# Kernel tuning notes

Measured on AMD Instinct MI355X. Metric: run time of the kernel, lower is better.

Reference implementation:

```python
import math
import jax, jax.numpy as jnp
import numpy as np

N, L, W = 64, 128, 256          # batch, num windows, window size
D, H, NL = 384, 8, 4            # d_model, heads, transformer layers
DFF = 1536
CH = [1, 4, 16, 64]             # conv channels (multiplier 4)
K = 7                            # conv kernel, pad 3, stride 1; pool k2 s2
LIN_IN = 64 * 32                # cnn_linear_size = 2048


def _pe(l, d):
    pos = np.arange(l)[:, None].astype(np.float32)
    i = np.arange(d // 2)[None, :].astype(np.float32)
    ang = pos / np.power(10000.0, 2.0 * i / d)
    pe = np.zeros((l, d), np.float32)
    pe[:, 0::2] = np.sin(ang)
    pe[:, 1::2] = np.cos(ang)
    return jnp.asarray(pe)


def _conv1d(x, w, b):
    y = jax.lax.conv_general_dilated(x, w, window_strides=(1,), padding=[(3, 3)],
                                     dimension_numbers=('NCH', 'OIH', 'NCH'))
    return y + b[None, :, None]


def _maxpool2(x):
    return jax.lax.reduce_window(x, -jnp.inf, jax.lax.max, (1, 1, 2), (1, 1, 2), 'VALID')


def _ln(x, g, b):
    m = x.mean(-1, keepdims=True)
    v = ((x - m) ** 2).mean(-1, keepdims=True)
    return (x - m) * jax.lax.rsqrt(v + 1e-5) * g + b


def setup_inputs() -> dict:
    key = jax.random.key(0)
    ks = iter(jax.random.split(key, 40))
    s = 0.02
    d = {'x': jax.random.normal(next(ks), (N, L, W), jnp.float32)}
    for i in range(3):
        d[f'conv_w{i}'] = jax.random.normal(next(ks), (CH[i + 1], CH[i], K), jnp.float32) * s
        d[f'conv_b{i}'] = jnp.zeros((CH[i + 1],), jnp.float32)
    d['embed_w'] = jax.random.normal(next(ks), (LIN_IN, D), jnp.float32) * s
    d['embed_b'] = jnp.zeros((D,), jnp.float32)
    for nm, sh in [('Wq', (NL, D, D)), ('Wk', (NL, D, D)), ('Wv', (NL, D, D)), ('Wo', (NL, D, D)),
                   ('W1', (NL, D, DFF)), ('W2', (NL, DFF, D))]:
        d[nm] = jax.random.normal(next(ks), sh, jnp.float32) * s
    for nm, sh in [('bq', (NL, D)), ('bk', (NL, D)), ('bv', (NL, D)), ('bo', (NL, D)),
                   ('b1', (NL, DFF)), ('b2', (NL, D))]:
        d[nm] = jnp.zeros(sh, jnp.float32)
    d['g1'] = jnp.ones((NL, D), jnp.float32); d['be1'] = jnp.zeros((NL, D), jnp.float32)
    d['g2'] = jnp.ones((NL, D), jnp.float32); d['be2'] = jnp.zeros((NL, D), jnp.float32)
    d['cls_w'] = jax.random.normal(next(ks), (D, 1), jnp.float32) * s
    d['cls_b'] = jnp.zeros((1,), jnp.float32)
    return d


def reference(x, conv_w0, conv_b0, conv_w1, conv_b1, conv_w2, conv_b2,
              embed_w, embed_b, Wq, bq, Wk, bk, Wv, bv, Wo, bo,
              W1, b1, W2, b2, g1, be1, g2, be2, cls_w, cls_b):
    n, l, w = x.shape
    # ---- CNN window encoder: each window -> d_model token ----
    h = x.reshape(n * l, 1, w)
    for cw, cb in ((conv_w0, conv_b0), (conv_w1, conv_b1), (conv_w2, conv_b2)):
        h = _maxpool2(jax.nn.relu(_conv1d(h, cw, cb)))
    h = h.reshape(n * l, -1)                      # (N*L, cnn_linear_size)
    h = jax.nn.relu(h @ embed_w + embed_b)        # (N*L, D)
    t = h.reshape(n, l, D) + _pe(l, D)
    # ---- transformer encoder (fast_transformers post-norm layers) ----
    E = D // H
    temp = 1.0 / math.sqrt(E)
    for i in range(Wq.shape[0]):
        q = (t @ Wq[i] + bq[i]).reshape(n, l, H, E)
        k = (t @ Wk[i] + bk[i]).reshape(n, l, H, E)
        v = (t @ Wv[i] + bv[i]).reshape(n, l, H, E)
        A = jax.nn.softmax(temp * jnp.einsum('nlhe,nshe->nhls', q, k), axis=-1)
        o = jnp.einsum('nhls,nshd->nlhd', A, v).reshape(n, l, D)
        t = _ln(t + o @ Wo[i] + bo[i], g1[i], be1[i])
        y = jax.nn.relu(t @ W1[i] + b1[i]) @ W2[i] + b2[i]
        t = _ln(t + y, g2[i], be2[i])
    # ---- classifier head: mean pool over windows -> logit ----
    return t.mean(axis=1) @ cls_w + cls_b          # (N, 1)
```

## Files before the change

### kernel.cpp

```cpp
#include <hip/hip_runtime.h>
#include <math.h>


typedef float f32x4 __attribute__((ext_vector_type(4)));
typedef short bf16x8 __attribute__((ext_vector_type(8)));
typedef short s16x4 __attribute__((ext_vector_type(4)));

__device__ __forceinline__ short f2bf(float f) {
    union { float f; unsigned u; } c; c.f = f;
    unsigned r = (c.u + 0x7FFFu + ((c.u >> 16) & 1u)) >> 16;
    return (short)r;
}
__device__ __forceinline__ float bf2f(short s) {
    union { unsigned u; float f; } c;
    c.u = ((unsigned)(unsigned short)s) << 16;
    return c.f;
}

__device__ __forceinline__ void gload_lds16(const void* g, void* l) {
    __builtin_amdgcn_global_load_lds(
        (const __attribute__((address_space(1))) unsigned int*)g,
        (__attribute__((address_space(3))) unsigned int*)l,
        16, 0, 0);
}

__global__ __launch_bounds__(256) void prep_kernel(
    const float* __restrict__ ew,
    const float* __restrict__ Wq, const float* __restrict__ Wk,
    const float* __restrict__ Wv, const float* __restrict__ Wo,
    const float* __restrict__ W1, const float* __restrict__ W2,
    const float* __restrict__ bq, const float* __restrict__ bk,
    const float* __restrict__ bv, const float* __restrict__ w2,
    short* __restrict__ ewT, short* __restrict__ WqkvT,
    short* __restrict__ WoT, short* __restrict__ W1T,
    short* __restrict__ W2T, float* __restrict__ pe,
    float* __restrict__ bqkv, short* __restrict__ w2T)
{
    __shared__ float tile[32][33];
    int id = blockIdx.x;
    int tid = threadIdx.x;
    int tx = tid & 31, ty = tid >> 5;

    const float* Wp;
    short* Wtp;
    int K, N, kb, nb;

    if (id < 768) {
        K = 2048; N = 384;
        kb = (id & 63) * 32; nb = (id >> 6) * 32;
        Wp = ew; Wtp = ewT;
    } else if (id < 2496) {
        int t = id - 768;
        int kbi = t % 12, nbi = (t / 12) % 12, z = t / 144;
        int layer = z / 3, which = z - layer * 3;
        K = 384; N = 384; kb = kbi * 32; nb = nbi * 32;
        Wp = (which == 0 ? Wq : (which == 1 ? Wk : Wv)) + (size_t)layer * 147456;
        Wtp = WqkvT + (size_t)layer * 442368 + (size_t)which * 147456;
    } else if (id < 3072) {
        int t = id - 2496;
        int kbi = t % 12, nbi = (t / 12) % 12, z = t / 144;
        K = 384; N = 384; kb = kbi * 32; nb = nbi * 32;
        Wp = Wo + (size_t)z * 147456; Wtp = WoT + (size_t)z * 147456;
    } else if (id < 5376) {
        int t = id - 3072;
        int kbi = t % 12, nbi = (t / 12) % 48, z = t / 576;
        K = 384; N = 1536; kb = kbi * 32; nb = nbi * 32;
        Wp = W1 + (size_t)z * 589824; Wtp = W1T + (size_t)z * 589824;
    } else if (id < 7680) {
        int t = id - 5376;
        int kbi = t % 48, nbi = (t / 48) % 12, z = t / 576;
        K = 1536; N = 384; kb = kbi * 32; nb = nbi * 32;
        Wp = W2 + (size_t)z * 589824; Wtp = W2T + (size_t)z * 589824;
    } else if (id < 7872) {
        int idx = (id - 7680) * 256 + tid;
        int l = idx / 384, d = idx - l * 384;
        int i2 = d >> 1;
        float ang = (float)l * expf(-(2.0f * (float)i2 / 384.0f) * 9.210340371976184f);
        pe[idx] = (d & 1) ? cosf(ang) : sinf(ang);
        return;
    } else if (id < 7890) {
        int idx = (id - 7872) * 256 + tid;
        int l = idx / 1152, j3 = idx - l * 1152;
        int which = j3 / 384, j = j3 - which * 384;
        const float* b = (which == 0 ? bq : (which == 1 ? bk : bv));
        bqkv[idx] = b[l * 384 + j];
        return;
    } else {
        int idx = (id - 7890) * 256 + tid;
        int c = idx >> 7, r = idx & 127;
        int pr = r >> 5, q = (r >> 3) & 3, j = r & 7;
        int ci = (q & 1) * 8 + j;
        int sft = 2 * pr + (q >> 1);
        w2T[idx] = (sft < 7) ? f2bf(w2[c * 112 + ci * 7 + sft]) : (short)0;
        return;
    }

    #pragma unroll
    for (int r = ty; r < 32; r += 8)
        tile[r][tx] = Wp[(size_t)(kb + r) * N + nb + tx];
    __syncthreads();
    #pragma unroll
    for (int r = ty; r < 32; r += 8)
        Wtp[(size_t)(nb + r) * K + kb + tx] = f2bf(tile[tx][r]);
}

__global__ __launch_bounds__(256, 4) void cnn_kernel(
    const float* __restrict__ x,
    const float* __restrict__ w0, const float* __restrict__ b0,
    const float* __restrict__ w1, const float* __restrict__ b1,
    const short* __restrict__ w2T, const float* __restrict__ b2,
    short* __restrict__ feat)
{
    __shared__ __align__(16) char smem[26880];
    float* xs  = (float*)smem;
    float* p0  = (float*)(smem + 4224);
    short* p1T = (short*)(smem + 13056);

    int tid = threadIdx.x;
    int w = tid >> 6, lane = tid & 63;
    size_t win = (size_t)blockIdx.x * 4 + w;
    int cq = lane >> 4, cl = lane & 15;

    float* xs_w = xs + w * 264;
    float* p0_w = p0 + w * 552;
    short* p1T_w = p1T + w * 1728;

    int ca = lane & 3;
    int cb = lane & 15, g = lane >> 4;
    float w0r[7], w1r[4][7];
    float b0r = b0[ca];
    float b1r = b1[cb];
    #pragma unroll
    for (int k = 0; k < 7; ++k) w0r[k] = w0[ca * 7 + k];
    #pragma unroll
    for (int ci = 0; ci < 4; ++ci)
        #pragma unroll
        for (int k = 0; k < 7; ++k) w1r[ci][k] = w1[(cb * 4 + ci) * 7 + k];

    {
        f32x4 v = *(const f32x4*)(x + win * 256 + lane * 4);
        *(f32x4*)&xs_w[4 + lane * 4] = v;
        if (lane < 2) *(f32x4*)&xs_w[lane * 260] = (f32x4){0.f, 0.f, 0.f, 0.f};
    }

    {
        int pa = lane >> 2;
        #pragma unroll
        for (int t2 = 0; t2 < 8; ++t2) {
            int pp = t2 * 16 + pa;
            float rv[9];
            #pragma unroll
            for (int u = 0; u < 9; ++u) rv[u] = xs_w[2 * pp + u + 1];
            float a0 = b0r, a1 = b0r;
            #pragma unroll
            for (int k = 0; k < 7; ++k) {
                a0 = fmaf(w0r[k], rv[k], a0);
                a1 = fmaf(w0r[k], rv[k + 1], a1);
            }
            p0_w[ca * 138 + pp + 3] = fmaxf(fmaxf(a0, a1), 0.f);
        }
        if (lane < 4) {
            p0_w[lane * 138 + 0] = 0.f;
            p0_w[lane * 138 + 1] = 0.f;
            p0_w[lane * 138 + 2] = 0.f;
            p0_w[lane * 138 + 131] = 0.f;
            p0_w[lane * 138 + 132] = 0.f;
            p0_w[lane * 138 + 133] = 0.f;
        }
    }

    #pragma unroll
    for (int cc = 0; cc < 4; ++cc) {
        int cci = (cc + g) & 3;
        int j0 = g * 32 + cci * 8;
        float acc[8];
        #pragma unroll
        for (int m = 0; m < 8; ++m) acc[m] = b1r;
        #pragma unroll
        for (int ci = 0; ci < 4; ++ci) {
            float rv[14];
            #pragma unroll
            for (int u = 0; u < 14; ++u) rv[u] = p0_w[ci * 138 + j0 + u];
            #pragma unroll
            for (int k = 0; k < 7; ++k) {
                float ww = w1r[ci][k];
                #pragma unroll
                for (int m = 0; m < 8; ++m) acc[m] = fmaf(ww, rv[m + k], acc[m]);
            }
        }
        int po = g * 16 + cci * 4;
        #pragma unroll
        for (int m = 0; m < 4; ++m)
            p1T_w[(3 + po + m) * 24 + cb] =
                f2bf(fmaxf(fmaxf(acc[2 * m], acc[2 * m + 1]), 0.f));
    }
    {
        int* pz = (int*)p1T_w;
        if (lane < 36) pz[lane] = 0;
        if (lane < 60) pz[804 + lane] = 0;
    }
    __syncthreads();

    f32x4 acc[4][4];
    #pragma unroll
    for (int v = 0; v < 4; ++v)
        #pragma unroll
        for (int mt = 0; mt < 4; ++mt)
            acc[v][mt] = (f32x4){0.f, 0.f, 0.f, 0.f};

    {
        const short* bpb = p1T + (w * 16 + cl + (cq >> 1)) * 24 + (cq & 1) * 8;
        #pragma unroll
        for (int pr = 0; pr < 4; ++pr) {
            bf16x8 bfr[4];
            #pragma unroll
            for (int v = 0; v < 4; ++v)
                bfr[v] = *(const bf16x8*)&bpb[v * 1728 + pr * 48];
            #pragma unroll
            for (int mt = 0; mt < 4; ++mt) {
                bf16x8 af = *(const bf16x8*)&w2T[(mt * 16 + cl) * 128 +
                                                 pr * 32 + cq * 8];
                #pragma unroll
                for (int v = 0; v < 4; ++v)
                    acc[v][mt] = __builtin_amdgcn_mfma_f32_16x16x32_bf16(
                        af, bfr[v], acc[v][mt], 0, 0, 0);
            }
        }
    }

    int iev = (w * 16 + cl) >> 1;
    #pragma unroll
    for (int v = 0; v < 4; ++v) {
        short* fp = feat + ((size_t)blockIdx.x * 4 + v) * 2048;
        #pragma unroll
        for (int mt = 0; mt < 4; ++mt) {
            #pragma unroll
            for (int rg = 0; rg < 4; ++rg) {
                float vv = acc[v][mt][rg];
                float v2 = __shfl_xor(vv, 1, 64);
                if ((cl & 1) == 0) {
                    int c = mt * 16 + cq * 4 + rg;
                    float pv = fmaxf(fmaxf(vv, v2) + b2[c], 0.f);
                    fp[c * 32 + iev] = f2bf(pv);
                }
            }
        }
    }
}

template <int EPI>
__global__ __launch_bounds__(256) void gemm_bf16(
    const short* __restrict__ A, const short* __restrict__ Bt,
    const float* __restrict__ bias, const float* __restrict__ resid,
    const float* __restrict__ pe, float* __restrict__ outF,
    short* __restrict__ outB, int M, int N, int K)
{
    __shared__ short As[2][128 * 64];
    __shared__ short Bs[2][64 * 64];
    int tid = threadIdx.x;
    int w = tid >> 6, lane = tid & 63;
    int wm = w >> 1, wn = w & 1;
    int m0 = blockIdx.y * 128, n0 = blockIdx.x * 64;

    int rl = lane >> 3, sl = lane & 7;
    int cb = sl ^ rl;
    const short* aptr[4];
    const short* bptr[2];
    int arow[4], brow[2];
    #pragma unroll
    for (int l = 0; l < 4; ++l) {
        arow[l] = l * 32 + w * 8;
        aptr[l] = A + (size_t)(m0 + arow[l] + rl) * K + cb * 8;
    }
    #pragma unroll
    for (int l = 0; l < 2; ++l) {
        brow[l] = l * 32 + w * 8;
        bptr[l] = Bt + (size_t)(n0 + brow[l] + rl) * K + cb * 8;
    }

    int cq = lane >> 4, cl = lane & 15;
    f32x4 acc[4][2];
    #pragma unroll
    for (int mt = 0; mt < 4; ++mt)
        #pragma unroll
        for (int nt = 0; nt < 2; ++nt)
            acc[mt][nt] = (f32x4){0.f, 0.f, 0.f, 0.f};

    #pragma unroll
    for (int l = 0; l < 4; ++l) { gload_lds16(aptr[l], &As[0][arow[l] * 64]); aptr[l] += 64; }
    #pragma unroll
    for (int l = 0; l < 2; ++l) { gload_lds16(bptr[l], &Bs[0][brow[l] * 64]); bptr[l] += 64; }
    __syncthreads();

    int nk = K >> 6;
    for (int k = 0; k < nk; ++k) {
        int cur = k & 1;
        if (k + 1 < nk) {
            #pragma unroll
            for (int l = 0; l < 4; ++l) { gload_lds16(aptr[l], &As[cur ^ 1][arow[l] * 64]); aptr[l] += 64; }
            #pragma unroll
            for (int l = 0; l < 2; ++l) { gload_lds16(bptr[l], &Bs[cur ^ 1][brow[l] * 64]); bptr[l] += 64; }
        }
        #pragma unroll
        for (int s = 0; s < 2; ++s) {
            bf16x8 afr[4], bfr[2];
            #pragma unroll
            for (int mt = 0; mt < 4; ++mt) {
                int r = wm * 64 + mt * 16 + cl;
                int slot = (s * 4 + cq) ^ (r & 7);
                afr[mt] = *(const bf16x8*)&As[cur][r * 64 + slot * 8];
            }
            #pragma unroll
            for (int nt = 0; nt < 2; ++nt) {
                int r = wn * 32 + nt * 16 + cl;
                int slot = (s * 4 + cq) ^ (r & 7);
                bfr[nt] = *(const bf16x8*)&Bs[cur][r * 64 + slot * 8];
            }
            #pragma unroll
            for (int mt = 0; mt < 4; ++mt)
                #pragma unroll
                for (int nt = 0; nt < 2; ++nt)
                    acc[mt][nt] = __builtin_amdgcn_mfma_f32_16x16x32_bf16(
                        afr[mt], bfr[nt], acc[mt][nt], 0, 0, 0);
        }
        __syncthreads();
    }

    #pragma unroll
    for (int mt = 0; mt < 4; ++mt) {
        #pragma unroll
        for (int nt = 0; nt < 2; ++nt) {
            int col = n0 + wn * 32 + nt * 16 + cl;
            float bb = bias[col];
            #pragma unroll
            for (int rg = 0; rg < 4; ++rg) {
                int row = m0 + wm * 64 + mt * 16 + cq * 4 + rg;
                float v = acc[mt][nt][rg] + bb;
                if (EPI & 1) v = fmaxf(v, 0.f);
                if (EPI & 4) v += pe[(row & 127) * 384 + col];
                if (EPI & 2) v += resid[(size_t)row * N + col];
                if (EPI & 8) outF[(size_t)row * N + col] = v;
                if (EPI & 16) outB[(size_t)row * N + col] = f2bf(v);
            }
        }
    }
}

__global__ __launch_bounds__(512) void gemm_ln(
    const short* __restrict__ A, const short* __restrict__ Bt,
    const float* __restrict__ bias, const float* resid,
    const float* __restrict__ g, const float* __restrict__ be,
    float* t, short* __restrict__ tb, int K)
{
    __shared__ __align__(16) char smem[106496];
    short* As0 = (short*)smem;
    short* Bs0 = (short*)(smem + 8192);

    int tid = threadIdx.x;
    int w = tid >> 6, lane = tid & 63;
    int m0 = blockIdx.x * 32;
    int rl = lane >> 3, sl = lane & 7;
    int cb = sl ^ rl;

    const short* aptr = A + (size_t)(m0 + (w & 3) * 8 + rl) * K + cb * 8;
    const short* bptr[6];
    #pragma unroll
    for (int l = 0; l < 6; ++l)
        bptr[l] = Bt + (size_t)(w * 48 + l * 8 + rl) * K + cb * 8;

    int cq = lane >> 4, cl = lane & 15;
    f32x4 acc[2][3];
    #pragma unroll
    for (int mt = 0; mt < 2; ++mt)
        #pragma unroll
        for (int nt = 0; nt < 3; ++nt)
            acc[mt][nt] = (f32x4){0.f, 0.f, 0.f, 0.f};

    if (w < 4) { gload_lds16(aptr, &As0[(w * 8) * 64]); aptr += 64; }
    #pragma unroll
    for (int l = 0; l < 6; ++l) {
        gload_lds16(bptr[l], &Bs0[(w * 48 + l * 8) * 64]);
        bptr[l] += 64;
    }
    __syncthreads();

    int nk = K >> 6;
    for (int k = 0; k < nk; ++k) {
        int cur = k & 1;
        if (k + 1 < nk) {
            if (w < 4) { gload_lds16(aptr, &As0[(cur ^ 1) * 2048 + (w * 8) * 64]); aptr += 64; }
            #pragma unroll
            for (int l = 0; l < 6; ++l) {
                gload_lds16(bptr[l], &Bs0[(cur ^ 1) * 24576 + (w * 48 + l * 8) * 64]);
                bptr[l] += 64;
            }
        }
        const short* As = As0 + cur * 2048;
        const short* Bs = Bs0 + cur * 24576;
        #pragma unroll
        for (int s = 0; s < 2; ++s) {
            bf16x8 afr[2], bfr[3];
            #pragma unroll
            for (int mt = 0; mt < 2; ++mt) {
                int r = mt * 16 + cl;
                int slot = (s * 4 + cq) ^ (r & 7);
                afr[mt] = *(const bf16x8*)&As[r * 64 + slot * 8];
            }
            #pragma unroll
            for (int nt = 0; nt < 3; ++nt) {
                int r = w * 48 + nt * 16 + cl;
                int slot = (s * 4 + cq) ^ (r & 7);
                bfr[nt] = *(const bf16x8*)&Bs[r * 64 + slot * 8];
            }
            #pragma unroll
            for (int mt = 0; mt < 2; ++mt)
                #pragma unroll
                for (int nt = 0; nt < 3; ++nt)
                    acc[mt][nt] = __builtin_amdgcn_mfma_f32_16x16x32_bf16(
                        afr[mt], bfr[nt], acc[mt][nt], 0, 0, 0);
        }
        __syncthreads();
    }

    float* yb = (float*)smem;
    #pragma unroll
    for (int mt = 0; mt < 2; ++mt) {
        #pragma unroll
        for (int nt = 0; nt < 3; ++nt) {
            int col = w * 48 + nt * 16 + cl;
            float bb = bias[col];
            #pragma unroll
            for (int rg = 0; rg < 4; ++rg) {
                int rloc = mt * 16 + cq * 4 + rg;
                yb[rloc * 388 + col] =
                    acc[mt][nt][rg] + bb + resid[(size_t)(m0 + rloc) * 384 + col];
            }
        }
    }
    __syncthreads();

    int rloc = tid >> 4, sub = tid & 15;
    f32x4 vals[6];
    float s = 0.f, s2 = 0.f;
    #pragma unroll
    for (int m = 0; m < 6; ++m) {
        f32x4 vv = *(const f32x4*)&yb[rloc * 388 + m * 64 + sub * 4];
        vals[m] = vv;
        #pragma unroll
        for (int j = 0; j < 4; ++j) {
            s += vv[j];
            s2 = fmaf(vv[j], vv[j], s2);
        }
    }
    s += __shfl_xor(s, 1, 64);  s2 += __shfl_xor(s2, 1, 64);
    s += __shfl_xor(s, 2, 64);  s2 += __shfl_xor(s2, 2, 64);
    s += __shfl_xor(s, 4, 64);  s2 += __shfl_xor(s2, 4, 64);
    s += __shfl_xor(s, 8, 64);  s2 += __shfl_xor(s2, 8, 64);
    float mean = s * (1.f / 384.f);
    float var = s2 * (1.f / 384.f) - mean * mean;
    float inv = rsqrtf(var + 1e-5f);

    size_t ro = (size_t)(m0 + rloc) * 384;
    #pragma unroll
    for (int m = 0; m < 6; ++m) {
        int c0 = m * 64 + sub * 4;
        f32x4 gg = *(const f32x4*)&g[c0];
        f32x4 bb = *(const f32x4*)&be[c0];
        f32x4 ov;
        s16x4 ob2;
        #pragma unroll
        for (int j = 0; j < 4; ++j) {
            float v = (vals[m][j] - mean) * inv * gg[j] + bb[j];
            ov[j] = v;
            ob2[j] = f2bf(v);
        }
        *(f32x4*)&t[ro + c0] = ov;
        *(s16x4*)&tb[ro + c0] = ob2;
    }
}

__global__ __launch_bounds__(512) void ffn_ln(
    const short* __restrict__ A,
    const short* __restrict__ W1t,
    const short* __restrict__ W2t,
    const float* __restrict__ b1,
    const float* __restrict__ bias2,
    const float* resid,
    const float* __restrict__ g, const float* __restrict__ be,
    float* t, short* __restrict__ tb)
{
    __shared__ __align__(16) char smem[126976];
    short* Ats = (short*)smem;
    short* WsA = (short*)(smem + 24576);
    short* WsB = (short*)(smem + 73728);
    short* Hs  = (short*)(smem + 122880);

    int tid = threadIdx.x;
    int w = tid >> 6, lane = tid & 63;
    int m0 = blockIdx.x * 32;
    int rl = lane >> 3, sl = lane & 7;
    int cb = sl ^ rl;
    int cq = lane >> 4, cl = lane & 15;
    int mt = w & 1, nth = w >> 1;

    if (w < 4) {
        #pragma unroll
        for (int kc = 0; kc < 6; ++kc)
            gload_lds16(A + (size_t)(m0 + w * 8 + rl) * 384 + kc * 64 + cb * 8,
                        &Ats[(kc * 32 + w * 8) * 64]);
    }
    #pragma unroll
    for (int kc = 0; kc < 6; ++kc)
        gload_lds16(W1t + (size_t)(w * 8 + rl) * 384 + kc * 64 + cb * 8,
                    &WsA[(kc * 64 + w * 8) * 64]);
    __syncthreads();

    f32x4 yacc[2][3];
    #pragma unroll
    for (int m2 = 0; m2 < 2; ++m2)
        #pragma unroll
        for (int nt = 0; nt < 3; ++nt)
            yacc[m2][nt] = (f32x4){0.f, 0.f, 0.f, 0.f};

    for (int c = 0; c < 24; ++c) {
        #pragma unroll
        for (int l = 0; l < 6; ++l)
            gload_lds16(W2t + (size_t)(w * 48 + l * 8 + rl) * 1536 + c * 64 + cb * 8,
                        &WsB[(w * 48 + l * 8) * 64]);

        f32x4 hacc = (f32x4){0.f, 0.f, 0.f, 0.f};
        #pragma unroll
        for (int kc = 0; kc < 6; ++kc) {
            #pragma unroll
            for (int s = 0; s < 2; ++s) {
                int ra = mt * 16 + cl;
                int sa = (s * 4 + cq) ^ (ra & 7);
                bf16x8 af = *(const bf16x8*)&Ats[(kc * 32 + ra) * 64 + sa * 8];
                int rb = nth * 16 + cl;
                int sb = (s * 4 + cq) ^ (rb & 7);
                bf16x8 bf = *(const bf16x8*)&WsA[(kc * 64 + rb) * 64 + sb * 8];
                hacc = __builtin_amdgcn_mfma_f32_16x16x32_bf16(af, bf, hacc, 0, 0, 0);
            }
        }
        {
            int lc = nth * 16 + cl;
            float bb = b1[c * 64 + lc];
            int sgrp = (lc >> 3);
            #pragma unroll
            for (int rg = 0; rg < 4; ++rg) {
                int row = mt * 16 + cq * 4 + rg;
                float v = fmaxf(hacc[rg] + bb, 0.f);
                Hs[row * 64 + (sgrp ^ (row & 7)) * 8 + (lc & 7)] = f2bf(v);
            }
        }
        __syncthreads();

        if (c + 1 < 24) {
            #pragma unroll
            for (int kc = 0; kc < 6; ++kc)
                gload_lds16(W1t + (size_t)((c + 1) * 64 + w * 8 + rl) * 384 + kc * 64 + cb * 8,
                            &WsA[(kc * 64 + w * 8) * 64]);
        }
        #pragma unroll
        for (int s = 0; s < 2; ++s) {
            bf16x8 haf[2], wbf[3];
            #pragma unroll
            for (int m2 = 0; m2 < 2; ++m2) {
                int r = m2 * 16 + cl;
                int slot = (s * 4 + cq) ^ (r & 7);
                haf[m2] = *(const bf16x8*)&Hs[r * 64 + slot * 8];
            }
            #pragma unroll
            for (int nt = 0; nt < 3; ++nt) {
                int r = w * 48 + nt * 16 + cl;
                int slot = (s * 4 + cq) ^ (r & 7);
                wbf[nt] = *(const bf16x8*)&WsB[r * 64 + slot * 8];
            }
            #pragma unroll
            for (int m2 = 0; m2 < 2; ++m2)
                #pragma unroll
                for (int nt = 0; nt < 3; ++nt)
                    yacc[m2][nt] = __builtin_amdgcn_mfma_f32_16x16x32_bf16(
                        haf[m2], wbf[nt], yacc[m2][nt], 0, 0, 0);
        }
        __syncthreads();
    }

    float* yb = (float*)smem;
    #pragma unroll
    for (int m2 = 0; m2 < 2; ++m2) {
        #pragma unroll
        for (int nt = 0; nt < 3; ++nt) {
            int col = w * 48 + nt * 16 + cl;
            float bb = bias2[col];
            #pragma unroll
            for (int rg = 0; rg < 4; ++rg) {
                int rloc = m2 * 16 + cq * 4 + rg;
                yb[rloc * 388 + col] =
                    yacc[m2][nt][rg] + bb + resid[(size_t)(m0 + rloc) * 384 + col];
            }
        }
    }
    __syncthreads();

    int rloc = tid >> 4, sub = tid & 15;
    f32x4 vals[6];
    float s = 0.f, s2 = 0.f;
    #pragma unroll
    for (int m = 0; m < 6; ++m) {
        f32x4 vv = *(const f32x4*)&yb[rloc * 388 + m * 64 + sub * 4];
        vals[m] = vv;
        #pragma unroll
        for (int j = 0; j < 4; ++j) {
            s += vv[j];
            s2 = fmaf(vv[j], vv[j], s2);
        }
    }
    s += __shfl_xor(s, 1, 64);  s2 += __shfl_xor(s2, 1, 64);
    s += __shfl_xor(s, 2, 64);  s2 += __shfl_xor(s2, 2, 64);
    s += __shfl_xor(s, 4, 64);  s2 += __shfl_xor(s2, 4, 64);
    s += __shfl_xor(s, 8, 64);  s2 += __shfl_xor(s2, 8, 64);
    float mean = s * (1.f / 384.f);
    float var = s2 * (1.f / 384.f) - mean * mean;
    float inv = rsqrtf(var + 1e-5f);

    size_t ro = (size_t)(m0 + rloc) * 384;
    #pragma unroll
    for (int m = 0; m < 6; ++m) {
        int c0 = m * 64 + sub * 4;
        f32x4 gg = *(const f32x4*)&g[c0];
        f32x4 bb = *(const f32x4*)&be[c0];
        f32x4 ov;
        s16x4 ob2;
        #pragma unroll
        for (int j = 0; j < 4; ++j) {
            float v = (vals[m][j] - mean) * inv * gg[j] + bb[j];
            ov[j] = v;
            ob2[j] = f2bf(v);
        }
        *(f32x4*)&t[ro + c0] = ov;
        *(s16x4*)&tb[ro + c0] = ob2;
    }
}

__global__ __launch_bounds__(256) void qkvattn_kernel(
    const short* __restrict__ A, const short* __restrict__ Bt,
    const float* __restrict__ bias, short* __restrict__ o)
{
    __shared__ __align__(16) char smem[76544];
    short* As0 = (short*)smem;
    short* Bs0 = (short*)(smem + 32768);
    short* Qs  = (short*)smem;
    short* Ks  = (short*)(smem + 14336);
    short* Vt  = (short*)(smem + 28672);
    short* P   = (short*)(smem + 41728);

    int tid = threadIdx.x;
    int w = tid >> 6, lane = tid & 63;
    int cq = lane >> 4, cl = lane & 15;
    int n = blockIdx.x >> 3, h = blockIdx.x & 7;
    int m0 = n * 128;

    int rl = lane >> 3, sl = lane & 7;
    int cb = sl ^ rl;
    const short* aptr[4];
    int arow[4];
    #pragma unroll
    for (int l = 0; l < 4; ++l) {
        arow[l] = l * 32 + w * 8;
        aptr[l] = A + (size_t)(m0 + arow[l] + rl) * 384 + cb * 8;
    }
    const short* bptr[5];
    int brow[5];
    #pragma unroll
    for (int l = 0; l < 5; ++l) {
        brow[l] = (l < 4) ? (l * 32 + w * 8) : (128 + w * 8);
        int r = brow[l] + rl;
        int g0 = (r >= 96) ? 2 : ((r >= 48) ? 1 : 0);
        int loc = r - g0 * 48;
        bptr[l] = Bt + (size_t)(g0 * 384 + h * 48 + loc) * 384 + cb * 8;
    }

    f32x4 acc[2][9];
    #pragma unroll
    for (int mt = 0; mt < 2; ++mt)
        #pragma unroll
        for (int nt = 0; nt < 9; ++nt)
            acc[mt][nt] = (f32x4){0.f, 0.f, 0.f, 0.f};

    #pragma unroll
    for (int l = 0; l < 4; ++l) { gload_lds16(aptr[l], &As0[arow[l] * 64]); aptr[l] += 64; }
    #pragma unroll
    for (int l = 0; l < 5; ++l) {
        if (l < 4 || w < 2) { gload_lds16(bptr[l], &Bs0[brow[l] * 64]); }
        bptr[l] += 64;
    }
    __syncthreads();

    for (int k = 0; k < 6; ++k) {
        int cur = k & 1;
        if (k + 1 < 6) {
            #pragma unroll
            for (int l = 0; l < 4; ++l) {
                gload_lds16(aptr[l], &As0[(cur ^ 1) * 8192 + arow[l] * 64]);
                aptr[l] += 64;
            }
            #pragma unroll
            for (int l = 0; l < 5; ++l) {
                if (l < 4 || w < 2)
                    gload_lds16(bptr[l], &Bs0[(cur ^ 1) * 9216 + brow[l] * 64]);
                bptr[l] += 64;
            }
        }
        const short* Asb = As0 + cur * 8192;
        const short* Bsb = Bs0 + cur * 9216;
        #pragma unroll
        for (int s = 0; s < 2; ++s) {
            bf16x8 afr[2], bfr[9];
            #pragma unroll
            for (int mt = 0; mt < 2; ++mt) {
                int r = w * 32 + mt * 16 + cl;
                int slot = (s * 4 + cq) ^ (r & 7);
                afr[mt] = *(const bf16x8*)&Asb[r * 64 + slot * 8];
            }
            #pragma unroll
            for (int nt = 0; nt < 9; ++nt) {
                int r = nt * 16 + cl;
                int slot = (s * 4 + cq) ^ (r & 7);
                bfr[nt] = *(const bf16x8*)&Bsb[r * 64 + slot * 8];
            }
            #pragma unroll
            for (int mt = 0; mt < 2; ++mt)
                #pragma unroll
                for (int nt = 0; nt < 9; ++nt)
                    acc[mt][nt] = __builtin_amdgcn_mfma_f32_16x16x32_bf16(
                        afr[mt], bfr[nt], acc[mt][nt], 0, 0, 0);
        }
        __syncthreads();
    }

    const float* bh = bias + h * 48;
    #pragma unroll
    for (int mt = 0; mt < 2; ++mt) {
        #pragma unroll
        for (int nt = 0; nt < 9; ++nt) {
            int grp = nt / 3;
            int col = (nt - grp * 3) * 16 + cl;
            float bb = bh[grp * 384 + col];
            if (grp == 2) {
                int row0 = w * 32 + mt * 16 + cq * 4;
                s16x4 pv;
                #pragma unroll
                for (int rg = 0; rg < 4; ++rg) pv[rg] = f2bf(acc[mt][nt][rg] + bb);
                *(s16x4*)&Vt[col * 136 + row0] = pv;
            } else {
                short* dst = (grp == 0) ? Qs : Ks;
                #pragma unroll
                for (int rg = 0; rg < 4; ++rg) {
                    int row = w * 32 + mt * 16 + cq * 4 + rg;
                    dst[row * 56 + col] = f2bf(acc[mt][nt][rg] + bb);
                }
            }
        }
    }
    __syncthreads();

    const bf16x8 zf = (bf16x8){0, 0, 0, 0, 0, 0, 0, 0};
    bf16x8 qf[2][2];
    #pragma unroll
    for (int mt = 0; mt < 2; ++mt) {
        int r = w * 32 + mt * 16 + cl;
        qf[mt][0] = *(const bf16x8*)&Qs[r * 56 + cq * 8];
        qf[mt][1] = (cq < 2) ? *(const bf16x8*)&Qs[r * 56 + 32 + cq * 8] : zf;
    }

    f32x4 sacc[2][8];
    #pragma unroll
    for (int mt = 0; mt < 2; ++mt)
        #pragma unroll
        for (int kt = 0; kt < 8; ++kt)
            sacc[mt][kt] = (f32x4){0.f, 0.f, 0.f, 0.f};

    #pragma unroll
    for (int kt = 0; kt < 8; ++kt) {
        int r = kt * 16 + cl;
        bf16x8 kf0 = *(const bf16x8*)&Ks[r * 56 + cq * 8];
        bf16x8 kf1 = (cq < 2) ? *(const bf16x8*)&Ks[r * 56 + 32 + cq * 8] : zf;
        #pragma unroll
        for (int mt = 0; mt < 2; ++mt) {
            sacc[mt][kt] = __builtin_amdgcn_mfma_f32_16x16x32_bf16(
                qf[mt][0], kf0, sacc[mt][kt], 0, 0, 0);
            sacc[mt][kt] = __builtin_amdgcn_mfma_f32_16x16x32_bf16(
                qf[mt][1], kf1, sacc[mt][kt], 0, 0, 0);
        }
    }

    const float temp = 0.14433756729740643f;
    short* Pw = P + w * 4352;
    float denom[2][4];
    #pragma unroll
    for (int mt = 0; mt < 2; ++mt) {
        #pragma unroll
        for (int rg = 0; rg < 4; ++rg) {
            float mx = sacc[mt][0][rg];
            #pragma unroll
            for (int kt = 1; kt < 8; ++kt) mx = fmaxf(mx, sacc[mt][kt][rg]);
            mx = fmaxf(mx, __shfl_xor(mx, 1, 64));
            mx = fmaxf(mx, __shfl_xor(mx, 2, 64));
            mx = fmaxf(mx, __shfl_xor(mx, 4, 64));
            mx = fmaxf(mx, __shfl_xor(mx, 8, 64));
            int row = mt * 16 + cq * 4 + rg;
            float se = 0.f;
            #pragma unroll
            for (int kt = 0; kt < 8; ++kt) {
                float p = __expf(temp * (sacc[mt][kt][rg] - mx));
                se += p;
                Pw[row * 136 + kt * 16 + cl] = f2bf(p);
            }
            se += __shfl_xor(se, 1, 64);
            se += __shfl_xor(se, 2, 64);
            se += __shfl_xor(se, 4, 64);
            se += __shfl_xor(se, 8, 64);
            denom[mt][rg] = se;
        }
    }

    f32x4 oacc[2][3];
    #pragma unroll
    for (int mt = 0; mt < 2; ++mt)
        #pragma unroll
        for (int nt = 0; nt < 3; ++nt)
            oacc[mt][nt] = (f32x4){0.f, 0.f, 0.f, 0.f};

    #pragma unroll
    for (int ks = 0; ks < 4; ++ks) {
        bf16x8 paf[2];
        #pragma unroll
        for (int mt = 0; mt < 2; ++mt)
            paf[mt] = *(const bf16x8*)&Pw[(mt * 16 + cl) * 136 + ks * 32 + cq * 8];
        #pragma unroll
        for (int nt = 0; nt < 3; ++nt) {
            bf16x8 vf = *(const bf16x8*)&Vt[(nt * 16 + cl) * 136 + ks * 32 + cq * 8];
            #pragma unroll
            for (int mt = 0; mt < 2; ++mt)
                oacc[mt][nt] = __builtin_amdgcn_mfma_f32_16x16x32_bf16(
                    paf[mt], vf, oacc[mt][nt], 0, 0, 0);
        }
    }

    #pragma unroll
    for (int mt = 0; mt < 2; ++mt) {
        #pragma unroll
        for (int rg = 0; rg < 4; ++rg) {
            float inv = 1.f / denom[mt][rg];
            int qrow = w * 32 + mt * 16 + cq * 4 + rg;
            short* op = o + ((size_t)n * 128 + qrow) * 384 + h * 48;
            #pragma unroll
            for (int nt = 0; nt < 3; ++nt)
                op[nt * 16 + cl] = f2bf(oacc[mt][nt][rg] * inv);
        }
    }
}

__global__ __launch_bounds__(384) void head_kernel(
    const float* __restrict__ t, const float* __restrict__ cls_w,
    const float* __restrict__ cls_b, float* __restrict__ out)
{
    int n = blockIdx.x, d = threadIdx.x;
    float s = 0.f;
    for (int l = 0; l < 128; ++l) s += t[((size_t)n * 128 + l) * 384 + d];
    float p = s * (1.f / 128.f) * cls_w[d];
    #pragma unroll
    for (int off = 32; off > 0; off >>= 1) p += __shfl_xor(p, off, 64);
    __shared__ float red[6];
    if ((threadIdx.x & 63) == 0) red[threadIdx.x >> 6] = p;
    __syncthreads();
    if (threadIdx.x == 0) {
        float tot = red[0] + red[1] + red[2] + red[3] + red[4] + red[5];
        out[n] = tot + cls_b[0];
    }
}

extern "C" void kernel_launch(void* const* d_in, const int* in_sizes, int n_in,
                              void* d_out, int out_size, void* d_ws, size_t ws_size,
                              hipStream_t stream) {
    (void)n_in; (void)out_size; (void)ws_size;
    const float* x   = (const float*)d_in[0];
    const float* cw0 = (const float*)d_in[1];
    const float* cb0 = (const float*)d_in[2];
    const float* cw1 = (const float*)d_in[3];
    const float* cb1 = (const float*)d_in[4];
    const float* cw2 = (const float*)d_in[5];
    const float* cb2 = (const float*)d_in[6];
    const float* ew  = (const float*)d_in[7];
    const float* eb  = (const float*)d_in[8];
    bool dict_order = (in_sizes[10] == 589824);
    const float *Wq, *Wk, *Wv, *Wo, *W1, *W2, *bq, *bk, *bv, *bo, *b1, *b2;
    if (dict_order) {
        Wq = (const float*)d_in[9];  Wk = (const float*)d_in[10];
        Wv = (const float*)d_in[11]; Wo = (const float*)d_in[12];
        W1 = (const float*)d_in[13]; W2 = (const float*)d_in[14];
        bq = (const float*)d_in[15]; bk = (const float*)d_in[16];
        bv = (const float*)d_in[17]; bo = (const float*)d_in[18];
        b1 = (const float*)d_in[19]; b2 = (const float*)d_in[20];
    } else {
        Wq = (const float*)d_in[9];  bq = (const float*)d_in[10];
        Wk = (const float*)d_in[11]; bk = (const float*)d_in[12];
        Wv = (const float*)d_in[13]; bv = (const float*)d_in[14];
        Wo = (const float*)d_in[15]; bo = (const float*)d_in[16];
        W1 = (const float*)d_in[17]; b1 = (const float*)d_in[18];
        W2 = (const float*)d_in[19]; b2 = (const float*)d_in[20];
    }
    const float* g1  = (const float*)d_in[21];
    const float* be1 = (const float*)d_in[22];
    const float* g2  = (const float*)d_in[23];
    const float* be2 = (const float*)d_in[24];
    const float* clw = (const float*)d_in[25];
    const float* clb = (const float*)d_in[26];

    char* wp = (char*)d_ws;
    float* pe    = (float*)wp; wp += 196608;
    short* featb = (short*)wp; wp += 33554432;
    float* t     = (float*)wp; wp += 12582912;
    short* tb    = (short*)wp; wp += 6291456;
    short* qkvb  = (short*)wp; wp += 18874368;
    short* ob    = (short*)wp; wp += 6291456;
    short* ewT   = (short*)wp; wp += 1572864;
    short* WqkvT = (short*)wp; wp += 3538944;
    short* WoT   = (short*)wp; wp += 1179648;
    short* W1T   = (short*)wp; wp += 4718592;
    short* W2T   = (short*)wp; wp += 4718592;
    float* bqkv  = (float*)wp; wp += 18432;
    short* w2T   = (short*)wp; wp += 16384;
    (void)qkvb;

    const int ROWS = 8192;

    prep_kernel<<<7922, 256, 0, stream>>>(ew, Wq, Wk, Wv, Wo, W1, W2,
                                          bq, bk, bv, cw2,
                                          ewT, WqkvT, WoT, W1T, W2T,
                                          pe, bqkv, w2T);
    cnn_kernel<<<2048, 256, 0, stream>>>(x, cw0, cb0, cw1, cb1, w2T, cb2, featb);

    gemm_bf16<29><<<dim3(6, 64), 256, 0, stream>>>(featb, ewT, eb, nullptr, pe,
                                                   t, tb, ROWS, 384, 2048);
    for (int i = 0; i < 4; ++i) {
        const short* WqkvTi = WqkvT + (size_t)i * 442368;
        const short* WoTi = WoT + (size_t)i * 147456;
        const short* W1Ti = W1T + (size_t)i * 589824;
        const short* W2Ti = W2T + (size_t)i * 589824;
        qkvattn_kernel<<<512, 256, 0, stream>>>(tb, WqkvTi, bqkv + i * 1152, ob);
        gemm_ln<<<256, 512, 0, stream>>>(ob, WoTi, bo + i * 384, t,
            g1 + i * 384, be1 + i * 384, t, tb, 384);
        ffn_ln<<<256, 512, 0, stream>>>(tb, W1Ti, W2Ti, b1 + i * 1536,
            b2 + i * 384, t, g2 + i * 384, be2 + i * 384, t, tb);
    }
    head_kernel<<<64, 384, 0, stream>>>(t, clw, clb, (float*)d_out);
}
```

Measured before the change: 573.5 us.

## Software-pipeline fused FFN kernel with multi-buffered weight tiles and register-held A

```diff
diff --git a/kernel.cpp b/kernel.cpp
--- a/kernel.cpp
+++ b/kernel.cpp
@@ -489,30 +489,48 @@
     const float* __restrict__ g, const float* __restrict__ be,
     float* t, short* __restrict__ tb)
 {
-    __shared__ __align__(16) char smem[126976];
-    short* Ats = (short*)smem;
-    short* WsA = (short*)(smem + 24576);
-    short* WsB = (short*)(smem + 73728);
+    __shared__ __align__(16) char smem[128000];
+    short* WsA = (short*)smem;
+    short* WsB = (short*)(smem + 49152);
     short* Hs  = (short*)(smem + 122880);
 
     int tid = threadIdx.x;
     int w = tid >> 6, lane = tid & 63;
     int m0 = blockIdx.x * 32;
-    int rl = lane >> 3, sl = lane & 7;
-    int cb = sl ^ rl;
     int cq = lane >> 4, cl = lane & 15;
-    int mt = w & 1, nth = w >> 1;
-
+    int rl8 = lane >> 3, sl8 = lane & 7;
+    int cb8 = sl8 ^ rl8;
+    int rl16 = lane >> 2, sl4 = lane & 3;
+    int cb4 = sl4 ^ ((rl16 >> 1) & 3);
+    int mt = w & 1, nt2 = (w >> 1) & 1;
+
+    bf16x8 afr[12];
     if (w < 4) {
+        const short* ap = A + (size_t)(m0 + mt * 16 + cl) * 384;
         #pragma unroll
         for (int kc = 0; kc < 6; ++kc)
-            gload_lds16(A + (size_t)(m0 + w * 8 + rl) * 384 + kc * 64 + cb * 8,
-                        &Ats[(kc * 32 + w * 8) * 64]);
-    }
-    #pragma unroll
-    for (int kc = 0; kc < 6; ++kc)
-        gload_lds16(W1t + (size_t)(w * 8 + rl) * 384 + kc * 64 + cb * 8,
-                    &WsA[(kc * 64 + w * 8) * 64]);
+            #pragma unroll
+            for (int s = 0; s < 2; ++s)
+                afr[kc * 2 + s] = *(const bf16x8*)(ap + kc * 64 + s * 32 + cq * 8);
+    }
+
+    auto issueLoads = [&](int cidx, int bufA, int bufB) {
+        #pragma unroll
+        for (int j = 0; j < 3; ++j) {
+            int idx = w * 3 + j;
+            int kc = idx >> 2, rgrp = idx & 3;
+            gload_lds16(W1t + (size_t)(cidx * 32 + rgrp * 8 + rl8) * 384 + kc * 64 + cb8 * 8,
+                        &WsA[bufA * 12288 + (kc * 32 + rgrp * 8) * 64]);
+        }
+        #pragma unroll
+        for (int j = 0; j < 3; ++j) {
+            int rgrp = w * 3 + j;
+            gload_lds16(W2t + (size_t)(rgrp * 16 + rl16) * 1536 + cidx * 32 + cb4 * 8,
+                        &WsB[bufB * 12288 + (rgrp * 16) * 32]);
+        }
+    };
+
+    issueLoads(0, 0, 0);
     __syncthreads();
 
     f32x4 yacc[2][3];
@@ -522,59 +540,20 @@
         for (int nt = 0; nt < 3; ++nt)
             yacc[m2][nt] = (f32x4){0.f, 0.f, 0.f, 0.f};
 
-    for (int c = 0; c < 24; ++c) {
-        #pragma unroll
-        for (int l = 0; l < 6; ++l)
-            gload_lds16(W2t + (size_t)(w * 48 + l * 8 + rl) * 1536 + c * 64 + cb * 8,
-                        &WsB[(w * 48 + l * 8) * 64]);
-
-        f32x4 hacc = (f32x4){0.f, 0.f, 0.f, 0.f};
-        #pragma unroll
-        for (int kc = 0; kc < 6; ++kc) {
-            #pragma unroll
-            for (int s = 0; s < 2; ++s) {
-                int ra = mt * 16 + cl;
-                int sa = (s * 4 + cq) ^ (ra & 7);
-                bf16x8 af = *(const bf16x8*)&Ats[(kc * 32 + ra) * 64 + sa * 8];
-                int rb = nth * 16 + cl;
-                int sb = (s * 4 + cq) ^ (rb & 7);
-                bf16x8 bf = *(const bf16x8*)&WsA[(kc * 64 + rb) * 64 + sb * 8];
-                hacc = __builtin_amdgcn_mfma_f32_16x16x32_bf16(af, bf, hacc, 0, 0, 0);
-            }
-        }
-        {
-            int lc = nth * 16 + cl;
-            float bb = b1[c * 64 + lc];
-            int sgrp = (lc >> 3);
-            #pragma unroll
-            for (int rg = 0; rg < 4; ++rg) {
-                int row = mt * 16 + cq * 4 + rg;
-                float v = fmaxf(hacc[rg] + bb, 0.f);
-                Hs[row * 64 + (sgrp ^ (row & 7)) * 8 + (lc & 7)] = f2bf(v);
-            }
-        }
-        __syncthreads();
-
-        if (c + 1 < 24) {
-            #pragma unroll
-            for (int kc = 0; kc < 6; ++kc)
-                gload_lds16(W1t + (size_t)((c + 1) * 64 + w * 8 + rl) * 384 + kc * 64 + cb * 8,
-                            &WsA[(kc * 64 + w * 8) * 64]);
-        }
-        #pragma unroll
-        for (int s = 0; s < 2; ++s) {
+    for (int c = 0; c < 48; ++c) {
+        if (c + 1 < 48) issueLoads(c + 1, (c + 1) & 1, (c + 1) % 3);
+
+        if (c > 0) {
+            int bBr = (c - 1) % 3, bHr = (c - 1) & 1;
             bf16x8 haf[2], wbf[3];
             #pragma unroll
-            for (int m2 = 0; m2 < 2; ++m2) {
-                int r = m2 * 16 + cl;
-                int slot = (s * 4 + cq) ^ (r & 7);
-                haf[m2] = *(const bf16x8*)&Hs[r * 64 + slot * 8];
-            }
+            for (int m2 = 0; m2 < 2; ++m2)
+                haf[m2] = *(const bf16x8*)&Hs[bHr * 1280 + (m2 * 16 + cl) * 40 + cq * 8];
             #pragma unroll
             for (int nt = 0; nt < 3; ++nt) {
                 int r = w * 48 + nt * 16 + cl;
-                int slot = (s * 4 + cq) ^ (r & 7);
-                wbf[nt] = *(const bf16x8*)&WsB[r * 64 + slot * 8];
+                int slot = cq ^ ((r >> 1) & 3);
+                wbf[nt] = *(const bf16x8*)&WsB[bBr * 12288 + r * 32 + slot * 8];
             }
             #pragma unroll
             for (int m2 = 0; m2 < 2; ++m2)
@@ -583,7 +562,49 @@
                     yacc[m2][nt] = __builtin_amdgcn_mfma_f32_16x16x32_bf16(
                         haf[m2], wbf[nt], yacc[m2][nt], 0, 0, 0);
         }
+
+        if (w < 4) {
+            int bA = c & 1, bH = c & 1;
+            f32x4 hacc = (f32x4){0.f, 0.f, 0.f, 0.f};
+            int rb = nt2 * 16 + cl;
+            #pragma unroll
+            for (int kc = 0; kc < 6; ++kc)
+                #pragma unroll
+                for (int s = 0; s < 2; ++s) {
+                    int slot = (s * 4 + cq) ^ (rb & 7);
+                    bf16x8 bf = *(const bf16x8*)&WsA[bA * 12288 + (kc * 32 + rb) * 64 + slot * 8];
+                    hacc = __builtin_amdgcn_mfma_f32_16x16x32_bf16(
+                        afr[kc * 2 + s], bf, hacc, 0, 0, 0);
+                }
+            int lc = nt2 * 16 + cl;
+            float bb = b1[c * 32 + lc];
+            #pragma unroll
+            for (int rg = 0; rg < 4; ++rg) {
+                int row = mt * 16 + cq * 4 + rg;
+                Hs[bH * 1280 + row * 40 + lc] = f2bf(fmaxf(hacc[rg] + bb, 0.f));
+            }
+        }
         __syncthreads();
+    }
+
+    {
+        int bBr = 47 % 3, bHr = 47 & 1;
+        bf16x8 haf[2], wbf[3];
+        #pragma unroll
+        for (int m2 = 0; m2 < 2; ++m2)
+            haf[m2] = *(const bf16x8*)&Hs[bHr * 1280 + (m2 * 16 + cl) * 40 + cq * 8];
+        #pragma unroll
+        for (int nt = 0; nt < 3; ++nt) {
+            int r = w * 48 + nt * 16 + cl;
+            int slot = cq ^ ((r >> 1) & 3);
+            wbf[nt] = *(const bf16x8*)&WsB[bBr * 12288 + r * 32 + slot * 8];
+        }
+        #pragma unroll
+        for (int m2 = 0; m2 < 2; ++m2)
+            #pragma unroll
+            for (int nt = 0; nt < 3; ++nt)
+                yacc[m2][nt] = __builtin_amdgcn_mfma_f32_16x16x32_bf16(
+                    haf[m2], wbf[nt], yacc[m2][nt], 0, 0, 0);
     }
 
     float* yb = (float*)smem;
```

Measured after the change: 627.1 us. +9.3%, slower.
